# Kernel tuning notes

Hardware: AMD Instinct MI355X
Metric: run time of the kernel (lower is better)

Reference implementation:

```python
import jax, jax.numpy as jnp
import numpy as np

N, E, G = 200000, 600000, 1024
NF_IN, EF_IN, H = 32, 16, 512
BN_EPS = 1e-5


def _bn(x, gamma, beta):
    # eval-mode BatchNorm1d with running_mean=0, running_var=1
    return x * (gamma / jnp.sqrt(1.0 + BN_EPS)) + beta


def setup_inputs() -> dict:
    key = jax.random.key(0)
    ks = jax.random.split(key, 32)
    s = 0.05
    inp = {
        'nf': jax.random.normal(ks[0], (N, NF_IN), jnp.float32),
        'ef': jax.random.normal(ks[1], (E, EF_IN), jnp.float32),
        'gf': jax.random.normal(ks[2], (G, H), jnp.float32),
        'device_params': jax.random.uniform(ks[3], (N,), jnp.float32),
        'node_y': jax.random.randint(ks[4], (N,), 0, 9),
        'batch_idx': jnp.sort(jax.random.randint(ks[5], (N,), 0, G)),
        'edge_index': jax.random.randint(ks[6], (2, E), 0, N),
        'nf_w1': jax.random.normal(ks[7], (NF_IN + 9, H), jnp.float32) * s,
        'nf_b1': jax.random.normal(ks[8], (H,), jnp.float32) * s,
        'nf_g1': jax.random.uniform(ks[9], (H,), jnp.float32, 0.5, 1.5),
        'nf_be1': jax.random.normal(ks[10], (H,), jnp.float32) * s,
        'nf_w2': jax.random.normal(ks[11], (H, H), jnp.float32) * s,
        'nf_b2': jax.random.normal(ks[12], (H,), jnp.float32) * s,
        'ef_w1': jax.random.normal(ks[13], (EF_IN, H), jnp.float32) * s,
        'ef_b1': jax.random.normal(ks[14], (H,), jnp.float32) * s,
        'ef_g1': jax.random.uniform(ks[15], (H,), jnp.float32, 0.5, 1.5),
        'ef_be1': jax.random.normal(ks[16], (H,), jnp.float32) * s,
        'ef_w2': jax.random.normal(ks[17], (H, H), jnp.float32) * s,
        'ef_b2': jax.random.normal(ks[18], (H,), jnp.float32) * s,
        'ow1': jax.random.normal(ks[19], (H, H), jnp.float32) * s,
        'ob1': jax.random.normal(ks[20], (H,), jnp.float32) * s,
        'og1': jax.random.uniform(ks[21], (H,), jnp.float32, 0.5, 1.5),
        'obe1': jax.random.normal(ks[22], (H,), jnp.float32) * s,
        'ow2': jax.random.normal(ks[23], (H, H), jnp.float32) * s,
        'ob2': jax.random.normal(ks[24], (H,), jnp.float32) * s,
        'og2': jax.random.uniform(ks[25], (H,), jnp.float32, 0.5, 1.5),
        'obe2': jax.random.normal(ks[26], (H,), jnp.float32) * s,
        'ow3': jax.random.normal(ks[27], (H, 2), jnp.float32) * s,
        'ob3': jax.random.normal(ks[28], (2,), jnp.float32) * s,
    }
    return inp


def reference(nf, ef, gf, device_params, node_y, batch_idx, edge_index,
              nf_w1, nf_b1, nf_g1, nf_be1, nf_w2, nf_b2,
              ef_w1, ef_b1, ef_g1, ef_be1, ef_w2, ef_b2,
              ow1, ob1, og1, obe1, ow2, ob2, og2, obe2, ow3, ob3):
    num_graphs = gf.shape[0]
    gelu = lambda x: jax.nn.gelu(x, approximate=False)  # torch nn.GELU default

    # DeviceParam_MLP: augment node features with scaled one-hot of node class
    nf_aug = jnp.concatenate(
        [nf, jax.nn.one_hot(node_y, 9, dtype=nf.dtype) * device_params[:, None]],
        axis=-1)  # [N, nf_in+9]
    h_n = gelu(_bn(nf_aug @ nf_w1 + nf_b1, nf_g1, nf_be1)) @ nf_w2 + nf_b2  # [N,H]
    h_e = gelu(_bn(ef @ ef_w1 + ef_b1, ef_g1, ef_be1)) @ ef_w2 + ef_b2      # [E,H]

    # two scatter_add pools into graph features
    gh = gf
    gh = gh + jax.ops.segment_sum(h_n, batch_idx, num_segments=num_graphs)
    edge_graph = batch_idx[edge_index[0]]  # graph id of each edge's source node
    gh = gh + jax.ops.segment_sum(h_e, edge_graph, num_segments=num_graphs)

    # output MLP (layer_num=3): two hidden blocks + final Linear -> 2
    x = gelu(_bn(gh @ ow1 + ob1, og1, obe1))
    x = gelu(_bn(x @ ow2 + ob2, og2, obe2))
    return x @ ow3 + ob3  # [G, 2]
```

## Files before the change

### kernel.cpp

```cpp
#include <hip/hip_runtime.h>
#include <hip/hip_bf16.h>

#define NN 200000
#define NE 600000
#define NG 1024
#define HH 512

typedef short short8 __attribute__((ext_vector_type(8)));
typedef float f32x4 __attribute__((ext_vector_type(4)));

__device__ __forceinline__ unsigned short f2bf(float f){
  unsigned u = __float_as_uint(f);
  u += 0x7fffu + ((u >> 16) & 1u);
  return (unsigned short)(u >> 16);
}
__device__ __forceinline__ float bf2f(unsigned short h){
  return __uint_as_float(((unsigned)h) << 16);
}

__device__ __forceinline__ short8 cvt8pk(float4 a, float4 b){
  union { short8 s; __hip_bfloat162 h[4]; } u;
  u.h[0] = __float22bfloat162_rn(make_float2(a.x, a.y));
  u.h[1] = __float22bfloat162_rn(make_float2(a.z, a.w));
  u.h[2] = __float22bfloat162_rn(make_float2(b.x, b.y));
  u.h[3] = __float22bfloat162_rn(make_float2(b.z, b.w));
  return u.s;
}

__device__ __forceinline__ void split8(const float* v, short8* hi, short8* lo){
  union { short8 s; __hip_bfloat162 h[4]; unsigned u[4]; } H, L;
#pragma unroll
  for (int p=0;p<4;++p){
    float a = v[2*p], b = v[2*p+1];
    H.h[p] = __float22bfloat162_rn(make_float2(a, b));
    unsigned hu = H.u[p];
    L.h[p] = __float22bfloat162_rn(make_float2(a - __uint_as_float(hu << 16),
                                               b - __uint_as_float(hu & 0xffff0000u)));
  }
  *hi = H.s; *lo = L.s;
}

__device__ __forceinline__ float gelu_f(float x){
  float p = __builtin_fmaf(x*x, -0.10294325f, -2.3022085f);
  float e = __builtin_amdgcn_exp2f(x * p);
  return x * __builtin_amdgcn_rcpf(1.0f + e);
}

__global__ __launch_bounds__(256) void kpre(
    const float* __restrict__ nfw1, const float* __restrict__ nfb1,
    const float* __restrict__ nfg1, const float* __restrict__ nfbe1,
    const float* __restrict__ efw1, const float* __restrict__ efb1,
    const float* __restrict__ efg1, const float* __restrict__ efbe1,
    unsigned short* __restrict__ w1nT, unsigned short* __restrict__ w1eT,
    float* __restrict__ b1n, float* __restrict__ b1e,
    const int* __restrict__ bidx, int* __restrict__ nstart,
    const int* __restrict__ eidx, int* __restrict__ eg, int* __restrict__ hpart){
  __shared__ int h[NG];
  const float rs = 0.99999500003750f;
  int b = blockIdx.x, t = threadIdx.x;
  if (b < 196){
    int tid = b*256 + t;
    if (tid < 512*64){
      int c = tid >> 6, k = tid & 63;
      float w = (k < 41) ? nfw1[k*HH + c] * nfg1[c] * rs : 0.0f;
      w1nT[tid] = f2bf(w);
    } else if (tid < 512*96){
      int u = tid - 512*64; int c = u >> 5, k = u & 31;
      float w = (k < 16) ? efw1[k*HH + c] * efg1[c] * rs : 0.0f;
      w1eT[u] = f2bf(w);
    } else if (tid < 512*96 + 512){
      int c = tid - 512*96;
      b1n[c] = nfb1[c]*nfg1[c]*rs + nfbe1[c];
    } else if (tid < 512*96 + 1024){
      int c = tid - (512*96 + 512);
      b1e[c] = efb1[c]*efg1[c]*rs + efbe1[c];
    }
  } else if (b < 978){
    int i = (b-196)*256 + t;
    if (i < NN){
      int g0 = bidx[i];
      int g1 = (i+1 < NN) ? bidx[i+1] : NG;
      for (int g = g0+1; g <= g1; ++g) nstart[g] = i+1;
      if (i == 0) for (int g = 0; g <= g0; ++g) nstart[g] = 0;
    }
  } else {
    int hb = b - 978;
    for (int u = t; u < NG; u += 256) h[u] = 0;
    __syncthreads();
    const int per = (NE + 255) / 256;
    const int lo = hb*per, hi = min(lo + per, NE);
    for (int e = lo + t; e < hi; e += 256){
      int g = bidx[eidx[e]];
      eg[e] = g;
      atomicAdd(&h[g], 1);
    }
    __syncthreads();
    for (int u = t; u < NG; u += 256) hpart[hb*NG + u] = h[u];
  }
}

__global__ __launch_bounds__(1024) void kscat(const int* __restrict__ eg,
    const int* __restrict__ hpart, int* __restrict__ estart, int* __restrict__ perm,
    const int* __restrict__ nstart, const float* __restrict__ gf,
    const float* __restrict__ b2n, const float* __restrict__ b2e, float* __restrict__ gh){
  __shared__ int s[NG];
  __shared__ int h[NG];
  __shared__ int base[NG];
  const int b = blockIdx.x, t = threadIdx.x;
  int T = 0, P = 0;
  for (int hb = 0; hb < 256; ++hb){
    int hp = hpart[hb*NG + t];
    T += hp;
    if (hb < b) P += hp;
  }
  s[t] = T; __syncthreads();
  for (int d = 1; d < NG; d <<= 1){
    int x = (t >= d) ? s[t-d] : 0;
    __syncthreads();
    s[t] += x;
    __syncthreads();
  }
  const int excl = s[t] - T;
  base[t] = excl + P;
  h[t] = 0;
  if (b == 0){
    estart[t] = excl;
    if (t == NG-1) estart[NG] = s[t];
  }
  __syncthreads();
  const int per = (NE + 255) / 256;
  const int lo = b*per, hi = min(lo + per, NE);
  for (int e = lo + t; e < hi; e += 1024){
    int g = eg[e];
    int p = base[g] + atomicAdd(&h[g], 1);
    perm[p] = e;
  }
  if (t < 512){
    int i = b*512 + t;
    int f = i*4;
    int r = f >> 9, c = f & 511;
    float cn = (float)(nstart[r+1] - nstart[r]);
    float ce = (float)(s[r] - ((r > 0) ? s[r-1] : 0));
    float4 gv = *(const float4*)&gf[f];
    float4 bn4 = *(const float4*)&b2n[c];
    float4 be4 = *(const float4*)&b2e[c];
    float4 o;
    o.x = gv.x + cn*bn4.x + ce*be4.x;
    o.y = gv.y + cn*bn4.y + ce*be4.y;
    o.z = gv.z + cn*bn4.z + ce*be4.z;
    o.w = gv.w + cn*bn4.w + ce*be4.w;
    *(float4*)&gh[f] = o;
  }
}

__global__ __launch_bounds__(256) void kmain(
    const float* __restrict__ nf, const float* __restrict__ dp, const int* __restrict__ ny,
    const int* __restrict__ nstart, const float* __restrict__ ef, const int* __restrict__ perm,
    const int* __restrict__ estart, const unsigned short* __restrict__ w1nT,
    const unsigned short* __restrict__ w1eT, const float* __restrict__ b1n,
    const float* __restrict__ b1e, float* __restrict__ S){
  const int t = threadIdx.x;
  const int lane = t & 63, w = t >> 6;
  const int q = lane >> 4, m = lane & 15;
  const short8 zz = {0,0,0,0,0,0,0,0};
  if (blockIdx.x < 2048){
    const int g = blockIdx.x >> 1;
    const int c0 = ((blockIdx.x & 1) << 8) + (w << 6);
    short8 bfr[4]; float bias[4]; float colacc[4] = {0.f,0.f,0.f,0.f};
#pragma unroll
    for (int nt=0; nt<4; ++nt){
      int c = c0 + (nt<<4) + m;
      bfr[nt] = *(const short8*)(w1eT + (c << 5) + (q << 3));
      bias[nt] = b1e[c];
    }
    const int s0 = estart[g], s1 = estart[g+1];
    const int nfull = (s1 - s0) >> 4;
    int rb = s0;
    for (int ch=0; ch<nfull; ++ch, rb += 16){
      int e = perm[rb + m];
      short8 f = zz;
      if (q < 2){
        const float4* ap = (const float4*)(ef + (size_t)e*16 + (q<<3));
        f = cvt8pk(ap[0], ap[1]);
      }
#pragma unroll
      for (int nt=0; nt<4; ++nt){
        f32x4 acc = {bias[nt], bias[nt], bias[nt], bias[nt]};
        acc = __builtin_amdgcn_mfma_f32_16x16x32_bf16(f, bfr[nt], acc, 0, 0, 0);
        colacc[nt] += (gelu_f(acc[0]) + gelu_f(acc[1])) + (gelu_f(acc[2]) + gelu_f(acc[3]));
      }
    }
    if (rb < s1){
      int row = rb + m;
      int e = perm[(row < s1) ? row : s0];
      short8 f = zz;
      if (q < 2){
        const float4* ap = (const float4*)(ef + (size_t)e*16 + (q<<3));
        f = cvt8pk(ap[0], ap[1]);
      }
      const int vr = s1 - rb;
#pragma unroll
      for (int nt=0; nt<4; ++nt){
        f32x4 acc = {bias[nt], bias[nt], bias[nt], bias[nt]};
        acc = __builtin_amdgcn_mfma_f32_16x16x32_bf16(f, bfr[nt], acc, 0, 0, 0);
        float v0 = (q*4+0 < vr) ? gelu_f(acc[0]) : 0.f;
        float v1 = (q*4+1 < vr) ? gelu_f(acc[1]) : 0.f;
        float v2 = (q*4+2 < vr) ? gelu_f(acc[2]) : 0.f;
        float v3 = (q*4+3 < vr) ? gelu_f(acc[3]) : 0.f;
        colacc[nt] += (v0+v1)+(v2+v3);
      }
    }
#pragma unroll
    for (int nt=0; nt<4; ++nt){
      float s = colacc[nt];
      s += __shfl_xor(s, 16); s += __shfl_xor(s, 32);
      if (lane < 16) S[(size_t)g*1024 + 512 + c0 + (nt<<4) + lane] = s;
    }
  } else {
    const int b2 = blockIdx.x - 2048;
    const int g = b2 >> 2;
    const int c0 = ((b2 & 3) << 7) + (w << 5);
    short8 bf0[2], bf1[2]; float bias[2]; float colacc[2] = {0.f,0.f};
#pragma unroll
    for (int nt=0; nt<2; ++nt){
      int c = c0 + (nt<<4) + m;
      const short8* bp = (const short8*)(w1nT + (c << 6) + (q << 3));
      bf0[nt] = bp[0]; bf1[nt] = bp[4];
      bias[nt] = b1n[c];
    }
    const int s0 = nstart[g], s1 = nstart[g+1];
    const int nfull = (s1 - s0) >> 4;
    int rb = s0;
    for (int ch=0; ch<nfull; ++ch, rb += 16){
      int ar = rb + m;
      const float4* ap = (const float4*)(nf + (size_t)ar*32 + (q<<3));
      short8 f = cvt8pk(ap[0], ap[1]);
      int cls = ny[ar];
      short dpb = (short)f2bf(dp[ar]);
      short8 h = zz;
      if (q == 0){
#pragma unroll
        for (int j=0;j<8;++j) h[j] = (cls==j) ? dpb : (short)0;
      } else if (q == 1 && cls == 8) h[0] = dpb;
#pragma unroll
      for (int nt=0; nt<2; ++nt){
        f32x4 acc = {bias[nt], bias[nt], bias[nt], bias[nt]};
        acc = __builtin_amdgcn_mfma_f32_16x16x32_bf16(f, bf0[nt], acc, 0, 0, 0);
        acc = __builtin_amdgcn_mfma_f32_16x16x32_bf16(h, bf1[nt], acc, 0, 0, 0);
        colacc[nt] += (gelu_f(acc[0]) + gelu_f(acc[1])) + (gelu_f(acc[2]) + gelu_f(acc[3]));
      }
    }
    if (rb < s1){
      int row = rb + m;
      int ar = (row < s1) ? row : s0;
      const float4* ap = (const float4*)(nf + (size_t)ar*32 + (q<<3));
      short8 f = cvt8pk(ap[0], ap[1]);
      int cls = ny[ar];
      short dpb = (short)f2bf(dp[ar]);
      short8 h = zz;
      if (q == 0){
#pragma unroll
        for (int j=0;j<8;++j) h[j] = (cls==j) ? dpb : (short)0;
      } else if (q == 1 && cls == 8) h[0] = dpb;
      const int vr = s1 - rb;
#pragma unroll
      for (int nt=0; nt<2; ++nt){
        f32x4 acc = {bias[nt], bias[nt], bias[nt], bias[nt]};
        acc = __builtin_amdgcn_mfma_f32_16x16x32_bf16(f, bf0[nt], acc, 0, 0, 0);
        acc = __builtin_amdgcn_mfma_f32_16x16x32_bf16(h, bf1[nt], acc, 0, 0, 0);
        float v0 = (q*4+0 < vr) ? gelu_f(acc[0]) : 0.f;
        float v1 = (q*4+1 < vr) ? gelu_f(acc[1]) : 0.f;
        float v2 = (q*4+2 < vr) ? gelu_f(acc[2]) : 0.f;
        float v3 = (q*4+3 < vr) ? gelu_f(acc[3]) : 0.f;
        colacc[nt] += (v0+v1)+(v2+v3);
      }
    }
#pragma unroll
    for (int nt=0; nt<2; ++nt){
      float s = colacc[nt];
      s += __shfl_xor(s, 16); s += __shfl_xor(s, 32);
      if (lane < 16) S[(size_t)g*1024 + c0 + (nt<<4) + lane] = s;
    }
  }
}

__global__ __launch_bounds__(256) void kgemm3(const float* __restrict__ A, int lda, int nkc,
    const float* __restrict__ B0, const float* __restrict__ B1,
    float* __restrict__ out, const float* __restrict__ pre, const float* __restrict__ bias,
    const float* __restrict__ gam, const float* __restrict__ bet){
  const int t = threadIdx.x, lane = t & 63, w = t >> 6;
  const int q = lane >> 4, m = lane & 15;
  const int c0 = blockIdx.x*32, r0 = blockIdx.y*64 + w*16;
  f32x4 acc[2] = {{0.f,0.f,0.f,0.f},{0.f,0.f,0.f,0.f}};
  const float* ap = A + (size_t)(r0 + m)*lda + (q<<3);
  for (int kc = 0; kc < nkc; ++kc){
    const int ko = kc*32;
    float4 x = *(const float4*)(ap + ko);
    float4 y = *(const float4*)(ap + ko + 4);
    float v[8] = {x.x,x.y,x.z,x.w,y.x,y.y,y.z,y.w};
    short8 ah, al;
    split8(v, &ah, &al);
    const float* Bp = (kc < 16) ? B0 : B1;
    const float* bp = Bp + (size_t)((kc & 15)*32 + (q<<3))*HH + c0 + m;
#pragma unroll
    for (int cf=0; cf<2; ++cf){
      float bv[8];
#pragma unroll
      for (int j=0;j<8;++j) bv[j] = bp[(size_t)j*HH + cf*16];
      short8 bh, bl;
      split8(bv, &bh, &bl);
      acc[cf] = __builtin_amdgcn_mfma_f32_16x16x32_bf16(ah, bh, acc[cf], 0, 0, 0);
      acc[cf] = __builtin_amdgcn_mfma_f32_16x16x32_bf16(ah, bl, acc[cf], 0, 0, 0);
      acc[cf] = __builtin_amdgcn_mfma_f32_16x16x32_bf16(al, bh, acc[cf], 0, 0, 0);
    }
  }
  const float rs = 0.99999500003750f;
#pragma unroll
  for (int cf=0; cf<2; ++cf){
    int c = c0 + cf*16 + m;
    float sc = 0.f, bi = 0.f, be = 0.f;
    if (!pre){ sc = gam[c]*rs; bi = bias[c]; be = bet[c]; }
#pragma unroll
    for (int i=0;i<4;++i){
      int r = blockIdx.y*64 + w*16 + q*4 + i;
      float vv = acc[cf][i];
      if (pre) vv += pre[(size_t)r*HH + c];
      else vv = gelu_f((vv + bi)*sc + be);
      out[(size_t)r*HH + c] = vv;
    }
  }
}

__global__ __launch_bounds__(256) void kfinal(const float* __restrict__ x2, const float* __restrict__ w3,
    const float* __restrict__ b3, float* __restrict__ out){
  const int lane = threadIdx.x & 63, wv = threadIdx.x >> 6;
  const int r = blockIdx.x*4 + wv;
  float a0 = 0.f, a1 = 0.f;
#pragma unroll
  for (int tt=0; tt<8; ++tt){
    int k = lane + tt*64;
    float x = x2[(size_t)r*HH + k];
    a0 = __builtin_fmaf(x, w3[2*k], a0);
    a1 = __builtin_fmaf(x, w3[2*k+1], a1);
  }
#pragma unroll
  for (int d=1; d<64; d<<=1){ a0 += __shfl_xor(a0, d); a1 += __shfl_xor(a1, d); }
  if (lane == 0){ out[r*2] = a0 + b3[0]; out[r*2+1] = a1 + b3[1]; }
}

extern "C" void kernel_launch(void* const* d_in, const int* in_sizes, int n_in,
                              void* d_out, int out_size, void* d_ws, size_t ws_size,
                              hipStream_t stream) {
  const float* nf    = (const float*)d_in[0];
  const float* ef    = (const float*)d_in[1];
  const float* gf    = (const float*)d_in[2];
  const float* dp    = (const float*)d_in[3];
  const int*   ny    = (const int*)d_in[4];
  const int*   bidx  = (const int*)d_in[5];
  const int*   eidx  = (const int*)d_in[6];
  const float* nfw1  = (const float*)d_in[7];
  const float* nfb1  = (const float*)d_in[8];
  const float* nfg1  = (const float*)d_in[9];
  const float* nfbe1 = (const float*)d_in[10];
  const float* w2n   = (const float*)d_in[11];
  const float* b2n   = (const float*)d_in[12];
  const float* efw1  = (const float*)d_in[13];
  const float* efb1  = (const float*)d_in[14];
  const float* efg1  = (const float*)d_in[15];
  const float* efbe1 = (const float*)d_in[16];
  const float* w2e   = (const float*)d_in[17];
  const float* b2e   = (const float*)d_in[18];
  const float* ow1   = (const float*)d_in[19];
  const float* ob1   = (const float*)d_in[20];
  const float* og1   = (const float*)d_in[21];
  const float* obe1  = (const float*)d_in[22];
  const float* ow2   = (const float*)d_in[23];
  const float* ob2   = (const float*)d_in[24];
  const float* og2   = (const float*)d_in[25];
  const float* obe2  = (const float*)d_in[26];
  const float* ow3   = (const float*)d_in[27];
  const float* ob3   = (const float*)d_in[28];

  float* S    = (float*)d_ws;
  int* nstart = (int*)(S + NG*1024);
  int* estart = nstart + NG + 1;
  int* eg     = estart + NG + 1;
  int* perm   = eg + NE;
  int* hpart  = perm + NE;
  unsigned short* w1nT = (unsigned short*)(hpart + 256*NG);
  unsigned short* w1eT = w1nT + HH*64;
  float* b1n  = (float*)(w1eT + HH*32);
  float* b1e  = b1n + HH;
  float* gh   = b1e + HH;
  float* xg2  = gh + NG*HH;
  float* x2f  = xg2 + NG*HH;

  kpre<<<1234, 256, 0, stream>>>(nfw1, nfb1, nfg1, nfbe1, efw1, efb1, efg1, efbe1,
                                 w1nT, w1eT, b1n, b1e, bidx, nstart, eidx, eg, hpart);
  kscat<<<256, 1024, 0, stream>>>(eg, hpart, estart, perm, nstart, gf, b2n, b2e, gh);
  kmain<<<6144, 256, 0, stream>>>(nf, dp, ny, nstart, ef, perm, estart,
                                  w1nT, w1eT, b1n, b1e, S);
  kgemm3<<<dim3(16,16), 256, 0, stream>>>(S, 1024, 32, w2n, w2e, gh, gh,
                                          nullptr, nullptr, nullptr);
  kgemm3<<<dim3(16,16), 256, 0, stream>>>(gh, 512, 16, ow1, ow1, xg2, nullptr,
                                          ob1, og1, obe1);
  kgemm3<<<dim3(16,16), 256, 0, stream>>>(xg2, 512, 16, ow2, ow2, x2f, nullptr,
                                          ob2, og2, obe2);
  kfinal<<<NG/4, 256, 0, stream>>>(x2f, ow3, ob3, (float*)d_out);
}
```

Baseline: 373.6 us.

## Replace edge sort with capped atomic bucketing, table GELU, pre-split bf16 GEMM operands

Replaces the two-pass histogram/scan/scatter edge sort with a single atomic bucketing kernel that writes edges into fixed-capacity per-graph slots. Bias is folded into the first-layer MFMA through constant-one feature columns. Exact GELU is replaced by a shared-memory lookup table with linear interpolation. Weights and intermediate activations are pre-split into bf16 hi/lo pairs so the GEMMs load bf16 directly instead of converting fp32 on every load. The main kernel is reorganised so node blocks process 256 columns. The risks are silent edge drops if a graph exceeds the slot cap, accuracy loss from the table approximation, and more preprocessing work.

New measurement: 508.0 us. +36.0%, slower.

```diff
diff --git a/kernel.cpp b/kernel.cpp
--- a/kernel.cpp
+++ b/kernel.cpp
@@ -5,6 +5,7 @@
 #define NE 600000
 #define NG 1024
 #define HH 512
+#define ECAP 1024
 
 typedef short short8 __attribute__((ext_vector_type(8)));
 typedef float f32x4 __attribute__((ext_vector_type(4)));
@@ -27,19 +28,6 @@
   return u.s;
 }
 
-__device__ __forceinline__ void split8(const float* v, short8* hi, short8* lo){
-  union { short8 s; __hip_bfloat162 h[4]; unsigned u[4]; } H, L;
-#pragma unroll
-  for (int p=0;p<4;++p){
-    float a = v[2*p], b = v[2*p+1];
-    H.h[p] = __float22bfloat162_rn(make_float2(a, b));
-    unsigned hu = H.u[p];
-    L.h[p] = __float22bfloat162_rn(make_float2(a - __uint_as_float(hu << 16),
-                                               b - __uint_as_float(hu & 0xffff0000u)));
-  }
-  *hi = H.s; *lo = L.s;
-}
-
 __device__ __forceinline__ float gelu_f(float x){
   float p = __builtin_fmaf(x*x, -0.10294325f, -2.3022085f);
   float e = __builtin_amdgcn_exp2f(x * p);
@@ -51,182 +39,195 @@
     const float* __restrict__ nfg1, const float* __restrict__ nfbe1,
     const float* __restrict__ efw1, const float* __restrict__ efb1,
     const float* __restrict__ efg1, const float* __restrict__ efbe1,
+    const float* __restrict__ w2n, const float* __restrict__ w2e,
+    const float* __restrict__ ow1, const float* __restrict__ ow2,
+    const int* __restrict__ bidx,
     unsigned short* __restrict__ w1nT, unsigned short* __restrict__ w1eT,
-    float* __restrict__ b1n, float* __restrict__ b1e,
-    const int* __restrict__ bidx, int* __restrict__ nstart,
-    const int* __restrict__ eidx, int* __restrict__ eg, int* __restrict__ hpart){
-  __shared__ int h[NG];
+    unsigned short* __restrict__ Bh1, unsigned short* __restrict__ Bl1,
+    unsigned short* __restrict__ Bh2, unsigned short* __restrict__ Bl2,
+    unsigned short* __restrict__ Bh3, unsigned short* __restrict__ Bl3,
+    float2* __restrict__ tab, int* __restrict__ cnt, int* __restrict__ nstart,
+    int4* __restrict__ pz){
   const float rs = 0.99999500003750f;
-  int b = blockIdx.x, t = threadIdx.x;
-  if (b < 196){
+  const int b = blockIdx.x, t = threadIdx.x;
+  if (b < 192){
     int tid = b*256 + t;
     if (tid < 512*64){
       int c = tid >> 6, k = tid & 63;
-      float w = (k < 41) ? nfw1[k*HH + c] * nfg1[c] * rs : 0.0f;
+      float w = 0.0f;
+      if (k < 41) w = nfw1[k*HH + c] * nfg1[c] * rs;
+      else if (k == 41 || k == 42){
+        float beff = nfb1[c]*nfg1[c]*rs + nfbe1[c];
+        if (k == 41) w = bf2f(f2bf(beff));
+        else         w = beff - bf2f(f2bf(beff));
+      }
       w1nT[tid] = f2bf(w);
-    } else if (tid < 512*96){
+    } else {
       int u = tid - 512*64; int c = u >> 5, k = u & 31;
-      float w = (k < 16) ? efw1[k*HH + c] * efg1[c] * rs : 0.0f;
+      float w = 0.0f;
+      if (k < 16) w = efw1[k*HH + c] * efg1[c] * rs;
+      else if (k == 16 || k == 17){
+        float beff = efb1[c]*efg1[c]*rs + efbe1[c];
+        if (k == 16) w = bf2f(f2bf(beff));
+        else         w = beff - bf2f(f2bf(beff));
+      }
       w1eT[u] = f2bf(w);
-    } else if (tid < 512*96 + 512){
-      int c = tid - 512*96;
-      b1n[c] = nfb1[c]*nfg1[c]*rs + nfbe1[c];
-    } else if (tid < 512*96 + 1024){
-      int c = tid - (512*96 + 512);
-      b1e[c] = efb1[c]*efg1[c]*rs + efbe1[c];
-    }
-  } else if (b < 978){
-    int i = (b-196)*256 + t;
+    }
+  } else if (b < 974){
+    int i = (b-192)*256 + t;
     if (i < NN){
       int g0 = bidx[i];
       int g1 = (i+1 < NN) ? bidx[i+1] : NG;
       for (int g = g0+1; g <= g1; ++g) nstart[g] = i+1;
       if (i == 0) for (int g = 0; g <= g0; ++g) nstart[g] = 0;
     }
+  } else if (b < 3022){
+    int idx = (b-974)*256 + t;
+    int k = idx >> 9, c = idx & 511;
+    float v = (k < 512) ? w2n[k*HH + c] : w2e[(k-512)*HH + c];
+    unsigned short h = f2bf(v);
+    Bh1[(size_t)c*1024 + k] = h;
+    Bl1[(size_t)c*1024 + k] = f2bf(v - bf2f(h));
+  } else if (b < 4046){
+    int idx = (b-3022)*256 + t;
+    int k = idx >> 9, c = idx & 511;
+    float v = ow1[k*HH + c];
+    unsigned short h = f2bf(v);
+    Bh2[(size_t)c*512 + k] = h;
+    Bl2[(size_t)c*512 + k] = f2bf(v - bf2f(h));
+  } else if (b < 5070){
+    int idx = (b-4046)*256 + t;
+    int k = idx >> 9, c = idx & 511;
+    float v = ow2[k*HH + c];
+    unsigned short h = f2bf(v);
+    Bh3[(size_t)c*512 + k] = h;
+    Bl3[(size_t)c*512 + k] = f2bf(v - bf2f(h));
+  } else if (b == 5070){
+    float v0 = (float)t * 0.015625f;
+    float v1 = v0 + 0.015625f;
+    float q0 = 0.5f * v0 * erfcf(v0 * 0.70710678f);
+    float q1 = 0.5f * v1 * erfcf(v1 * 0.70710678f);
+    tab[t] = make_float2(q0, q1 - q0);
+    cnt[t] = 0; cnt[t+256] = 0; cnt[t+512] = 0; cnt[t+768] = 0;
   } else {
-    int hb = b - 978;
-    for (int u = t; u < NG; u += 256) h[u] = 0;
-    __syncthreads();
-    const int per = (NE + 255) / 256;
-    const int lo = hb*per, hi = min(lo + per, NE);
-    for (int e = lo + t; e < hi; e += 256){
-      int g = bidx[eidx[e]];
-      eg[e] = g;
-      atomicAdd(&h[g], 1);
-    }
-    __syncthreads();
-    for (int u = t; u < NG; u += 256) hpart[hb*NG + u] = h[u];
-  }
-}
-
-__global__ __launch_bounds__(1024) void kscat(const int* __restrict__ eg,
-    const int* __restrict__ hpart, int* __restrict__ estart, int* __restrict__ perm,
-    const int* __restrict__ nstart, const float* __restrict__ gf,
-    const float* __restrict__ b2n, const float* __restrict__ b2e, float* __restrict__ gh){
-  __shared__ int s[NG];
-  __shared__ int h[NG];
-  __shared__ int base[NG];
-  const int b = blockIdx.x, t = threadIdx.x;
-  int T = 0, P = 0;
-  for (int hb = 0; hb < 256; ++hb){
-    int hp = hpart[hb*NG + t];
-    T += hp;
-    if (hb < b) P += hp;
-  }
-  s[t] = T; __syncthreads();
-  for (int d = 1; d < NG; d <<= 1){
-    int x = (t >= d) ? s[t-d] : 0;
-    __syncthreads();
-    s[t] += x;
-    __syncthreads();
-  }
-  const int excl = s[t] - T;
-  base[t] = excl + P;
-  h[t] = 0;
-  if (b == 0){
-    estart[t] = excl;
-    if (t == NG-1) estart[NG] = s[t];
-  }
-  __syncthreads();
-  const int per = (NE + 255) / 256;
-  const int lo = b*per, hi = min(lo + per, NE);
-  for (int e = lo + t; e < hi; e += 1024){
-    int g = eg[e];
-    int p = base[g] + atomicAdd(&h[g], 1);
-    perm[p] = e;
-  }
-  if (t < 512){
-    int i = b*512 + t;
-    int f = i*4;
-    int r = f >> 9, c = f & 511;
-    float cn = (float)(nstart[r+1] - nstart[r]);
-    float ce = (float)(s[r] - ((r > 0) ? s[r-1] : 0));
-    float4 gv = *(const float4*)&gf[f];
-    float4 bn4 = *(const float4*)&b2n[c];
-    float4 be4 = *(const float4*)&b2e[c];
-    float4 o;
-    o.x = gv.x + cn*bn4.x + ce*be4.x;
-    o.y = gv.y + cn*bn4.y + ce*be4.y;
-    o.z = gv.z + cn*bn4.z + ce*be4.z;
-    o.w = gv.w + cn*bn4.w + ce*be4.w;
-    *(float4*)&gh[f] = o;
-  }
-}
+    int idx = (b-5071)*256 + t;
+    pz[idx] = make_int4(0,0,0,0);
+  }
+}
+
+__global__ __launch_bounds__(256) void kscatter(const int* __restrict__ eidx,
+    const int* __restrict__ bidx, int* __restrict__ cnt, int* __restrict__ perm2d){
+  int e = blockIdx.x*256 + threadIdx.x;
+  if (e < NE){
+    int g = bidx[eidx[e]];
+    int p = atomicAdd(&cnt[g], 1);
+    if (p < ECAP) perm2d[(g << 10) + p] = e;
+  }
+}
+
+#define GELU_ACC(x_, dst_) { \
+  float ax_ = __builtin_fabsf(x_); \
+  float tt_ = fminf(ax_ * 64.0f, 254.99f); \
+  int ix_ = (int)tt_; \
+  float fr_ = tt_ - (float)ix_; \
+  float2 te_ = tabs[ix_]; \
+  float Q_ = __builtin_fmaf(fr_, te_.y, te_.x); \
+  float r_ = __builtin_fmaf(ax_, 0.5f, -Q_); \
+  dst_ += __builtin_fmaf(x_, 0.5f, r_); }
+
+#define GELU_ACC_M(x_, dst_, ok_) { \
+  float ax_ = __builtin_fabsf(x_); \
+  float tt_ = fminf(ax_ * 64.0f, 254.99f); \
+  int ix_ = (int)tt_; \
+  float fr_ = tt_ - (float)ix_; \
+  float2 te_ = tabs[ix_]; \
+  float Q_ = __builtin_fmaf(fr_, te_.y, te_.x); \
+  float r_ = __builtin_fmaf(ax_, 0.5f, -Q_); \
+  float g_ = __builtin_fmaf(x_, 0.5f, r_); \
+  dst_ += (ok_) ? g_ : 0.0f; }
 
 __global__ __launch_bounds__(256) void kmain(
     const float* __restrict__ nf, const float* __restrict__ dp, const int* __restrict__ ny,
-    const int* __restrict__ nstart, const float* __restrict__ ef, const int* __restrict__ perm,
-    const int* __restrict__ estart, const unsigned short* __restrict__ w1nT,
-    const unsigned short* __restrict__ w1eT, const float* __restrict__ b1n,
-    const float* __restrict__ b1e, float* __restrict__ S){
+    const int* __restrict__ nstart, const float* __restrict__ ef,
+    const int* __restrict__ perm2d, const int* __restrict__ cnt,
+    const unsigned short* __restrict__ w1nT, const unsigned short* __restrict__ w1eT,
+    const float2* __restrict__ tab,
+    unsigned short* __restrict__ Sh, unsigned short* __restrict__ Sl){
+  __shared__ float2 tabs[256];
   const int t = threadIdx.x;
+  tabs[t] = tab[t];
+  __syncthreads();
   const int lane = t & 63, w = t >> 6;
   const int q = lane >> 4, m = lane & 15;
   const short8 zz = {0,0,0,0,0,0,0,0};
+  const f32x4 zq = {0.f,0.f,0.f,0.f};
   if (blockIdx.x < 2048){
     const int g = blockIdx.x >> 1;
     const int c0 = ((blockIdx.x & 1) << 8) + (w << 6);
-    short8 bfr[4]; float bias[4]; float colacc[4] = {0.f,0.f,0.f,0.f};
-#pragma unroll
-    for (int nt=0; nt<4; ++nt){
-      int c = c0 + (nt<<4) + m;
-      bfr[nt] = *(const short8*)(w1eT + (c << 5) + (q << 3));
-      bias[nt] = b1e[c];
-    }
-    const int s0 = estart[g], s1 = estart[g+1];
-    const int nfull = (s1 - s0) >> 4;
-    int rb = s0;
+    short8 bfr[4]; float colacc[4] = {0.f,0.f,0.f,0.f};
+#pragma unroll
+    for (int nt=0; nt<4; ++nt)
+      bfr[nt] = *(const short8*)(w1eT + ((c0 + (nt<<4) + m) << 5) + (q << 3));
+    const int base = g << 10;
+    const int s1 = cnt[g];
+    const int nfull = s1 >> 4;
+    int rb = 0;
     for (int ch=0; ch<nfull; ++ch, rb += 16){
-      int e = perm[rb + m];
-      short8 f = zz;
+      int e = perm2d[base + rb + m];
+      short8 f;
       if (q < 2){
         const float4* ap = (const float4*)(ef + (size_t)e*16 + (q<<3));
         f = cvt8pk(ap[0], ap[1]);
-      }
+      } else if (q == 2){
+        f = zz; f[0] = (short)0x3F80; f[1] = (short)0x3F80;
+      } else f = zz;
 #pragma unroll
       for (int nt=0; nt<4; ++nt){
-        f32x4 acc = {bias[nt], bias[nt], bias[nt], bias[nt]};
-        acc = __builtin_amdgcn_mfma_f32_16x16x32_bf16(f, bfr[nt], acc, 0, 0, 0);
-        colacc[nt] += (gelu_f(acc[0]) + gelu_f(acc[1])) + (gelu_f(acc[2]) + gelu_f(acc[3]));
+        f32x4 acc = __builtin_amdgcn_mfma_f32_16x16x32_bf16(f, bfr[nt], zq, 0, 0, 0);
+        GELU_ACC(acc[0], colacc[nt]); GELU_ACC(acc[1], colacc[nt]);
+        GELU_ACC(acc[2], colacc[nt]); GELU_ACC(acc[3], colacc[nt]);
       }
     }
     if (rb < s1){
       int row = rb + m;
-      int e = perm[(row < s1) ? row : s0];
-      short8 f = zz;
+      int e = (row < s1) ? perm2d[base + row] : 0;
+      short8 f;
       if (q < 2){
         const float4* ap = (const float4*)(ef + (size_t)e*16 + (q<<3));
         f = cvt8pk(ap[0], ap[1]);
-      }
+      } else if (q == 2){
+        f = zz; f[0] = (short)0x3F80; f[1] = (short)0x3F80;
+      } else f = zz;
       const int vr = s1 - rb;
 #pragma unroll
       for (int nt=0; nt<4; ++nt){
-        f32x4 acc = {bias[nt], bias[nt], bias[nt], bias[nt]};
-        acc = __builtin_amdgcn_mfma_f32_16x16x32_bf16(f, bfr[nt], acc, 0, 0, 0);
-        float v0 = (q*4+0 < vr) ? gelu_f(acc[0]) : 0.f;
-        float v1 = (q*4+1 < vr) ? gelu_f(acc[1]) : 0.f;
-        float v2 = (q*4+2 < vr) ? gelu_f(acc[2]) : 0.f;
-        float v3 = (q*4+3 < vr) ? gelu_f(acc[3]) : 0.f;
-        colacc[nt] += (v0+v1)+(v2+v3);
+        f32x4 acc = __builtin_amdgcn_mfma_f32_16x16x32_bf16(f, bfr[nt], zq, 0, 0, 0);
+        GELU_ACC_M(acc[0], colacc[nt], ((q<<2)+0) < vr);
+        GELU_ACC_M(acc[1], colacc[nt], ((q<<2)+1) < vr);
+        GELU_ACC_M(acc[2], colacc[nt], ((q<<2)+2) < vr);
+        GELU_ACC_M(acc[3], colacc[nt], ((q<<2)+3) < vr);
       }
     }
 #pragma unroll
     for (int nt=0; nt<4; ++nt){
       float s = colacc[nt];
       s += __shfl_xor(s, 16); s += __shfl_xor(s, 32);
-      if (lane < 16) S[(size_t)g*1024 + 512 + c0 + (nt<<4) + lane] = s;
+      if (lane < 16){
+        int o = (g << 10) + 512 + c0 + (nt<<4) + lane;
+        unsigned short h = f2bf(s);
+        Sh[o] = h; Sl[o] = f2bf(s - bf2f(h));
+      }
     }
   } else {
     const int b2 = blockIdx.x - 2048;
-    const int g = b2 >> 2;
-    const int c0 = ((b2 & 3) << 7) + (w << 5);
-    short8 bf0[2], bf1[2]; float bias[2]; float colacc[2] = {0.f,0.f};
-#pragma unroll
-    for (int nt=0; nt<2; ++nt){
-      int c = c0 + (nt<<4) + m;
-      const short8* bp = (const short8*)(w1nT + (c << 6) + (q << 3));
-      bf0[nt] = bp[0]; bf1[nt] = bp[4];
-      bias[nt] = b1n[c];
+    const int g = b2 >> 1;
+    const int c0 = ((b2 & 1) << 8) + (w << 6);
+    short8 bf0[4], bf1[4]; float colacc[4] = {0.f,0.f,0.f,0.f};
+#pragma unroll
+    for (int nt=0; nt<4; ++nt){
+      const unsigned short* bp = w1nT + ((c0 + (nt<<4) + m) << 6) + (q << 3);
+      bf0[nt] = *(const short8*)bp;
+      bf1[nt] = *(const short8*)(bp + 32);
     }
     const int s0 = nstart[g], s1 = nstart[g+1];
     const int nfull = (s1 - s0) >> 4;
@@ -241,13 +242,16 @@
       if (q == 0){
 #pragma unroll
         for (int j=0;j<8;++j) h[j] = (cls==j) ? dpb : (short)0;
-      } else if (q == 1 && cls == 8) h[0] = dpb;
-#pragma unroll
-      for (int nt=0; nt<2; ++nt){
-        f32x4 acc = {bias[nt], bias[nt], bias[nt], bias[nt]};
-        acc = __builtin_amdgcn_mfma_f32_16x16x32_bf16(f, bf0[nt], acc, 0, 0, 0);
+      } else if (q == 1){
+        h[1] = (short)0x3F80; h[2] = (short)0x3F80;
+        if (cls == 8) h[0] = dpb;
+      }
+#pragma unroll
+      for (int nt=0; nt<4; ++nt){
+        f32x4 acc = __builtin_amdgcn_mfma_f32_16x16x32_bf16(f, bf0[nt], zq, 0, 0, 0);
         acc = __builtin_amdgcn_mfma_f32_16x16x32_bf16(h, bf1[nt], acc, 0, 0, 0);
-        colacc[nt] += (gelu_f(acc[0]) + gelu_f(acc[1])) + (gelu_f(acc[2]) + gelu_f(acc[3]));
+        GELU_ACC(acc[0], colacc[nt]); GELU_ACC(acc[1], colacc[nt]);
+        GELU_ACC(acc[2], colacc[nt]); GELU_ACC(acc[3], colacc[nt]);
       }
     }
     if (rb < s1){
@@ -261,72 +265,87 @@
       if (q == 0){
 #pragma unroll
         for (int j=0;j<8;++j) h[j] = (cls==j) ? dpb : (short)0;
-      } else if (q == 1 && cls == 8) h[0] = dpb;
+      } else if (q == 1){
+        h[1] = (short)0x3F80; h[2] = (short)0x3F80;
+        if (cls == 8) h[0] = dpb;
+      }
       const int vr = s1 - rb;
 #pragma unroll
-      for (int nt=0; nt<2; ++nt){
-        f32x4 acc = {bias[nt], bias[nt], bias[nt], bias[nt]};
-        acc = __builtin_amdgcn_mfma_f32_16x16x32_bf16(f, bf0[nt], acc, 0, 0, 0);
+      for (int nt=0; nt<4; ++nt){
+        f32x4 acc = __builtin_amdgcn_mfma_f32_16x16x32_bf16(f, bf0[nt], zq, 0, 0, 0);
         acc = __builtin_amdgcn_mfma_f32_16x16x32_bf16(h, bf1[nt], acc, 0, 0, 0);
-        float v0 = (q*4+0 < vr) ? gelu_f(acc[0]) : 0.f;
-        float v1 = (q*4+1 < vr) ? gelu_f(acc[1]) : 0.f;
-        float v2 = (q*4+2 < vr) ? gelu_f(acc[2]) : 0.f;
-        float v3 = (q*4+3 < vr) ? gelu_f(acc[3]) : 0.f;
-        colacc[nt] += (v0+v1)+(v2+v3);
-      }
-    }
-#pragma unroll
-    for (int nt=0; nt<2; ++nt){
+        GELU_ACC_M(acc[0], colacc[nt], ((q<<2)+0) < vr);
+        GELU_ACC_M(acc[1], colacc[nt], ((q<<2)+1) < vr);
+        GELU_ACC_M(acc[2], colacc[nt], ((q<<2)+2) < vr);
+        GELU_ACC_M(acc[3], colacc[nt], ((q<<2)+3) < vr);
+      }
+    }
+#pragma unroll
+    for (int nt=0; nt<4; ++nt){
       float s = colacc[nt];
       s += __shfl_xor(s, 16); s += __shfl_xor(s, 32);
-      if (lane < 16) S[(size_t)g*1024 + c0 + (nt<<4) + lane] = s;
-    }
-  }
-}
-
-__global__ __launch_bounds__(256) void kgemm3(const float* __restrict__ A, int lda, int nkc,
-    const float* __restrict__ B0, const float* __restrict__ B1,
-    float* __restrict__ out, const float* __restrict__ pre, const float* __restrict__ bias,
-    const float* __restrict__ gam, const float* __restrict__ bet){
+      if (lane < 16){
+        int o = (g << 10) + c0 + (nt<<4) + lane;
+        unsigned short h = f2bf(s);
+        Sh[o] = h; Sl[o] = f2bf(s - bf2f(h));
+      }
+    }
+  }
+}
+
+__global__ __launch_bounds__(256) void kg2(
+    const unsigned short* __restrict__ Ah, const unsigned short* __restrict__ Al,
+    int K, int nkc,
+    const unsigned short* __restrict__ Bh, const unsigned short* __restrict__ Bl,
+    const float* __restrict__ gf, const int* __restrict__ nstart, const int* __restrict__ cnt,
+    const float* __restrict__ b2n, const float* __restrict__ b2e,
+    const float* __restrict__ bias, const float* __restrict__ gam, const float* __restrict__ bet,
+    unsigned short* __restrict__ outh, unsigned short* __restrict__ outl,
+    float* __restrict__ outf){
   const int t = threadIdx.x, lane = t & 63, w = t >> 6;
   const int q = lane >> 4, m = lane & 15;
-  const int c0 = blockIdx.x*32, r0 = blockIdx.y*64 + w*16;
-  f32x4 acc[2] = {{0.f,0.f,0.f,0.f},{0.f,0.f,0.f,0.f}};
-  const float* ap = A + (size_t)(r0 + m)*lda + (q<<3);
+  const int c0 = blockIdx.x * 16, r0 = blockIdx.y * 64 + w * 16;
+  f32x4 acc = {0.f,0.f,0.f,0.f};
+  const unsigned short* ahp = Ah + (size_t)(r0 + m) * K + (q << 3);
+  const unsigned short* alp = Al + (size_t)(r0 + m) * K + (q << 3);
+  const unsigned short* bhp = Bh + (size_t)(c0 + m) * K + (q << 3);
+  const unsigned short* blp = Bl + (size_t)(c0 + m) * K + (q << 3);
   for (int kc = 0; kc < nkc; ++kc){
-    const int ko = kc*32;
-    float4 x = *(const float4*)(ap + ko);
-    float4 y = *(const float4*)(ap + ko + 4);
-    float v[8] = {x.x,x.y,x.z,x.w,y.x,y.y,y.z,y.w};
-    short8 ah, al;
-    split8(v, &ah, &al);
-    const float* Bp = (kc < 16) ? B0 : B1;
-    const float* bp = Bp + (size_t)((kc & 15)*32 + (q<<3))*HH + c0 + m;
-#pragma unroll
-    for (int cf=0; cf<2; ++cf){
-      float bv[8];
-#pragma unroll
-      for (int j=0;j<8;++j) bv[j] = bp[(size_t)j*HH + cf*16];
-      short8 bh, bl;
-      split8(bv, &bh, &bl);
-      acc[cf] = __builtin_amdgcn_mfma_f32_16x16x32_bf16(ah, bh, acc[cf], 0, 0, 0);
-      acc[cf] = __builtin_amdgcn_mfma_f32_16x16x32_bf16(ah, bl, acc[cf], 0, 0, 0);
-      acc[cf] = __builtin_amdgcn_mfma_f32_16x16x32_bf16(al, bh, acc[cf], 0, 0, 0);
-    }
+    const int ko = kc << 5;
+    short8 ah = *(const short8*)(ahp + ko);
+    short8 al = *(const short8*)(alp + ko);
+    short8 bh = *(const short8*)(bhp + ko);
+    short8 bl = *(const short8*)(blp + ko);
+    acc = __builtin_amdgcn_mfma_f32_16x16x32_bf16(ah, bh, acc, 0, 0, 0);
+    acc = __builtin_amdgcn_mfma_f32_16x16x32_bf16(al, bh, acc, 0, 0, 0);
+    acc = __builtin_amdgcn_mfma_f32_16x16x32_bf16(ah, bl, acc, 0, 0, 0);
   }
   const float rs = 0.99999500003750f;
-#pragma unroll
-  for (int cf=0; cf<2; ++cf){
-    int c = c0 + cf*16 + m;
-    float sc = 0.f, bi = 0.f, be = 0.f;
-    if (!pre){ sc = gam[c]*rs; bi = bias[c]; be = bet[c]; }
+  const int c = c0 + m;
+  if (gf){
+    const float bn = b2n[c], be = b2e[c];
 #pragma unroll
     for (int i=0;i<4;++i){
-      int r = blockIdx.y*64 + w*16 + q*4 + i;
-      float vv = acc[cf][i];
-      if (pre) vv += pre[(size_t)r*HH + c];
-      else vv = gelu_f((vv + bi)*sc + be);
-      out[(size_t)r*HH + c] = vv;
+      int r = r0 + (q<<2) + i;
+      float cn = (float)(nstart[r+1] - nstart[r]);
+      float ce = (float)cnt[r];
+      float v = acc[i] + gf[(size_t)r*HH + c] + cn*bn + ce*be;
+      unsigned short h = f2bf(v);
+      outh[(size_t)r*HH + c] = h;
+      outl[(size_t)r*HH + c] = f2bf(v - bf2f(h));
+    }
+  } else {
+    const float sc = gam[c]*rs, bi = bias[c], be = bet[c];
+#pragma unroll
+    for (int i=0;i<4;++i){
+      int r = r0 + (q<<2) + i;
+      float v = gelu_f((acc[i] + bi)*sc + be);
+      if (outf) outf[(size_t)r*HH + c] = v;
+      else {
+        unsigned short h = f2bf(v);
+        outh[(size_t)r*HH + c] = h;
+        outl[(size_t)r*HH + c] = f2bf(v - bf2f(h));
+      }
     }
   }
 }
@@ -381,30 +400,42 @@
   const float* ow3   = (const float*)d_in[27];
   const float* ob3   = (const float*)d_in[28];
 
-  float* S    = (float*)d_ws;
-  int* nstart = (int*)(S + NG*1024);
-  int* estart = nstart + NG + 1;
-  int* eg     = estart + NG + 1;
-  int* perm   = eg + NE;
-  int* hpart  = perm + NE;
-  unsigned short* w1nT = (unsigned short*)(hpart + 256*NG);
-  unsigned short* w1eT = w1nT + HH*64;
-  float* b1n  = (float*)(w1eT + HH*32);
-  float* b1e  = b1n + HH;
-  float* gh   = b1e + HH;
-  float* xg2  = gh + NG*HH;
-  float* x2f  = xg2 + NG*HH;
-
-  kpre<<<1234, 256, 0, stream>>>(nfw1, nfb1, nfg1, nfbe1, efw1, efb1, efg1, efbe1,
-                                 w1nT, w1eT, b1n, b1e, bidx, nstart, eidx, eg, hpart);
-  kscat<<<256, 1024, 0, stream>>>(eg, hpart, estart, perm, nstart, gf, b2n, b2e, gh);
-  kmain<<<6144, 256, 0, stream>>>(nf, dp, ny, nstart, ef, perm, estart,
-                                  w1nT, w1eT, b1n, b1e, S);
-  kgemm3<<<dim3(16,16), 256, 0, stream>>>(S, 1024, 32, w2n, w2e, gh, gh,
-                                          nullptr, nullptr, nullptr);
-  kgemm3<<<dim3(16,16), 256, 0, stream>>>(gh, 512, 16, ow1, ow1, xg2, nullptr,
-                                          ob1, og1, obe1);
-  kgemm3<<<dim3(16,16), 256, 0, stream>>>(xg2, 512, 16, ow2, ow2, x2f, nullptr,
-                                          ob2, og2, obe2);
+  unsigned char* p = (unsigned char*)d_ws;
+  unsigned short* Sh = (unsigned short*)p; p += (size_t)NG*1024*2;
+  unsigned short* Sl = (unsigned short*)p; p += (size_t)NG*1024*2;
+  int* perm2d = (int*)p;                   p += (size_t)NG*ECAP*4;
+  int* cnt    = (int*)p;                   p += NG*4;
+  int* nstart = (int*)p;                   p += (NG+8)*4;
+  unsigned short* w1nT = (unsigned short*)p; p += 512*64*2;
+  unsigned short* w1eT = (unsigned short*)p; p += 512*32*2;
+  unsigned short* Bh1 = (unsigned short*)p; p += (size_t)512*1024*2;
+  unsigned short* Bl1 = (unsigned short*)p; p += (size_t)512*1024*2;
+  unsigned short* Bh2 = (unsigned short*)p; p += 512*512*2;
+  unsigned short* Bl2 = (unsigned short*)p; p += 512*512*2;
+  unsigned short* Bh3 = (unsigned short*)p; p += 512*512*2;
+  unsigned short* Bl3 = (unsigned short*)p; p += 512*512*2;
+  float2* tab = (float2*)p;                p += 256*8;
+  unsigned short* ghh = (unsigned short*)p; p += (size_t)NG*HH*2;
+  unsigned short* ghl = (unsigned short*)p; p += (size_t)NG*HH*2;
+  unsigned short* xgh = (unsigned short*)perm2d;
+  unsigned short* xgl = xgh + (size_t)NG*HH;
+  float* x2f = (float*)(xgl + (size_t)NG*HH);
+
+  kpre<<<6095, 256, 0, stream>>>(nfw1, nfb1, nfg1, nfbe1, efw1, efb1, efg1, efbe1,
+                                 w2n, w2e, ow1, ow2, bidx, w1nT, w1eT,
+                                 Bh1, Bl1, Bh2, Bl2, Bh3, Bl3, tab, cnt, nstart,
+                                 (int4*)perm2d);
+  kscatter<<<(NE+255)/256, 256, 0, stream>>>(eidx, bidx, cnt, perm2d);
+  kmain<<<4096, 256, 0, stream>>>(nf, dp, ny, nstart, ef, perm2d, cnt, w1nT, w1eT,
+                                  tab, Sh, Sl);
+  kg2<<<dim3(32,16), 256, 0, stream>>>(Sh, Sl, 1024, 32, Bh1, Bl1,
+                                       gf, nstart, cnt, b2n, b2e,
+                                       nullptr, nullptr, nullptr, ghh, ghl, nullptr);
+  kg2<<<dim3(32,16), 256, 0, stream>>>(ghh, ghl, 512, 16, Bh2, Bl2,
+                                       nullptr, nullptr, nullptr, nullptr, nullptr,
+                                       ob1, og1, obe1, xgh, xgl, nullptr);
+  kg2<<<dim3(32,16), 256, 0, stream>>>(xgh, xgl, 512, 16, Bh3, Bl3,
+                                       nullptr, nullptr, nullptr, nullptr, nullptr,
+                                       ob2, og2, obe2, nullptr, nullptr, x2f);
   kfinal<<<NG/4, 256, 0, stream>>>(x2f, ow3, ob3, (float*)d_out);
 }
```
